# Kernel tuning notes

Measured on AMD Instinct MI355X. Metric: run time of the kernel, lower is better.

The kernel has to match this reference:

```python
import jax, jax.numpy as jnp
import numpy as np


def _hausdorff(x, y):
    # x, y: [B, C, N, D] point sets per (batch, channel); rows are points.
    x2 = jnp.sum(x * x, axis=-1)                       # [B, C, N]
    y2 = jnp.sum(y * y, axis=-1)                       # [B, C, M]
    xy = jnp.einsum('bcnd,bcmd->bcnm', x, y)           # [B, C, N, M]
    d2 = x2[..., :, None] + y2[..., None, :] - 2.0 * xy
    d = jnp.sqrt(jnp.maximum(d2, 0.0))                 # Euclidean distances
    d_fwd = jnp.max(jnp.min(d, axis=-1), axis=-1)      # max_n min_m, [B, C]
    d_bwd = jnp.max(jnp.min(d, axis=-2), axis=-1)      # max_m min_n, [B, C]
    return jnp.maximum(d_fwd, d_bwd)                   # symmetric Hausdorff [B, C]


def setup_inputs() -> dict:
    key = jax.random.key(0)
    k1, k2 = jax.random.split(key)
    B, C, H, W = 8, 3, 1024, 1024
    inp = jax.random.normal(k1, (B, C, H, W), dtype=jnp.float32)
    tgt = jax.random.normal(k2, (B, C, H, W), dtype=jnp.float32)
    return {'input': inp, 'target': tgt}


def reference(input, target):
    h = _hausdorff(input, target)        # [B, C]
    # original: sum_i mean_c(h[i]) / B == mean over (B, C)
    return jnp.mean(h)
```

## Files before the change

kernel.cpp:

```cpp
#include <hip/hip_runtime.h>
#include <math.h>

constexpr int BC = 24;
constexpr int N  = 1024;
constexpr int D  = 1024;
constexpr int TILE = 128;
constexpr int SKF = 40;

typedef short short8 __attribute__((ext_vector_type(8)));
typedef float f32x4  __attribute__((ext_vector_type(4)));

#define FINF 3.402823466e+38f


__device__ inline unsigned pk_bf16(float a, float b) {
    unsigned ua = __float_as_uint(a) + 0x8000u;
    unsigned ub = __float_as_uint(b) + 0x8000u;
    return __builtin_amdgcn_perm(ub, ua, 0x07060302);
}

__global__ __launch_bounds__(256) void prep_kernel(const float* __restrict__ X,
                                                   const float* __restrict__ Y,
                                                   unsigned short* __restrict__ Xsw,
                                                   unsigned short* __restrict__ Ysw,
                                                   float* __restrict__ xn,
                                                   float* __restrict__ yn) {
    int wave = threadIdx.x >> 6, lane = threadIdx.x & 63;
    int gtile = blockIdx.x * 4 + wave;
    bool isY = gtile >= 49152;
    int tile = isY ? gtile - 49152 : gtile;
    int bc = tile >> 11;
    int rk = tile & 2047;
    int R = rk >> 5, K = rk & 31;
    int r16 = lane & 15, quad = lane >> 4;

    const float* src = (isY ? Y : X) + ((size_t)bc * N + R * 16 + r16) * D + K * 32 + quad * 8;
    float4 a = *(const float4*)src;
    float4 b = *(const float4*)(src + 4);

    uint4 pk;
    pk.x = pk_bf16(a.x, a.y); pk.y = pk_bf16(a.z, a.w);
    pk.z = pk_bf16(b.x, b.y); pk.w = pk_bf16(b.z, b.w);
    unsigned short* dst = (isY ? Ysw : Xsw) + (size_t)tile * 512 + lane * 8;
    *(uint4*)dst = pk;

    float s = a.x * a.x + a.y * a.y + a.z * a.z + a.w * a.w
            + b.x * b.x + b.y * b.y + b.z * b.z + b.w * b.w;
    s += __shfl_xor(s, 16, 64);
    s += __shfl_xor(s, 32, 64);
    if (quad == 0)
        atomicAdd(&(isY ? yn : xn)[bc * N + R * 16 + r16], s);
}

__global__ __launch_bounds__(256) void tile_bf16_kernel(const unsigned short* __restrict__ Xsw,
                                                        const unsigned short* __restrict__ Ysw,
                                                        const float* __restrict__ xn,
                                                        const float* __restrict__ yn,
                                                        unsigned* __restrict__ rowmin,
                                                        unsigned* __restrict__ colmin) {
    int id = blockIdx.x;
    int xcd = id & 7, q = id >> 3;
    int bc = xcd * 3 + (q >> 6);
    int txy = q & 63;
    int tm = txy & 7, tn = txy >> 3;

    int wave = threadIdx.x >> 6, lane = threadIdx.x & 63;
    int wr = wave >> 1, wc = wave & 1;
    int quad = lane >> 4, tx = lane & 15;

    const unsigned short* Xb = Xsw + (size_t)bc * 2048 * 512;
    const unsigned short* Yb = Ysw + (size_t)bc * 2048 * 512;
    const unsigned short* ax = Xb + (size_t)(tn * 8 + wr * 4) * 32 * 512 + lane * 8;
    const unsigned short* by = Yb + (size_t)(tm * 8 + wc * 4) * 32 * 512 + lane * 8;

    f32x4 acc[4][4];
    #pragma unroll
    for (int i = 0; i < 4; i++)
        #pragma unroll
        for (int j = 0; j < 4; j++) acc[i][j] = (f32x4)0.f;

    short8 af[2][4], bg[2][4];
    #pragma unroll
    for (int mi = 0; mi < 4; mi++) {
        af[0][mi] = *(const short8*)(ax + mi * 16384);
        bg[0][mi] = *(const short8*)(by + mi * 16384);
    }
    #pragma unroll 2
    for (int d = 0; d < 32; d++) {
        int cur = d & 1, nxt = cur ^ 1;
        if (d < 31) {
            #pragma unroll
            for (int mi = 0; mi < 4; mi++) {
                af[nxt][mi] = *(const short8*)(ax + mi * 16384 + (d + 1) * 512);
                bg[nxt][mi] = *(const short8*)(by + mi * 16384 + (d + 1) * 512);
            }
        }
        #pragma unroll
        for (int mi = 0; mi < 4; mi++)
            #pragma unroll
            for (int mj = 0; mj < 4; mj++)
                acc[mi][mj] = __builtin_amdgcn_mfma_f32_16x16x32_bf16(af[cur][mi], bg[cur][mj], acc[mi][mj], 0, 0, 0);
    }

    int rbase = bc * N + tn * TILE + wr * 64;
    int cbase = bc * N + tm * TILE + wc * 64;
    float xnr[4][4], ynr[4];
    #pragma unroll
    for (int mi = 0; mi < 4; mi++)
        #pragma unroll
        for (int r = 0; r < 4; r++) xnr[mi][r] = xn[rbase + mi * 16 + quad * 4 + r];
    #pragma unroll
    for (int mj = 0; mj < 4; mj++) ynr[mj] = yn[cbase + mj * 16 + tx];

    float rmin[4][4], cmin[4];
    #pragma unroll
    for (int mi = 0; mi < 4; mi++)
        #pragma unroll
        for (int r = 0; r < 4; r++) rmin[mi][r] = FINF;
    #pragma unroll
    for (int mj = 0; mj < 4; mj++) cmin[mj] = FINF;

    #pragma unroll
    for (int mi = 0; mi < 4; mi++)
        #pragma unroll
        for (int mj = 0; mj < 4; mj++)
            #pragma unroll
            for (int r = 0; r < 4; r++) {
                float d2 = fmaxf(xnr[mi][r] + ynr[mj] - 2.f * acc[mi][mj][r], 0.f);
                rmin[mi][r] = fminf(rmin[mi][r], d2);
                cmin[mj]    = fminf(cmin[mj], d2);
            }

    #pragma unroll
    for (int m = 1; m < 16; m <<= 1)
        #pragma unroll
        for (int mi = 0; mi < 4; mi++)
            #pragma unroll
            for (int r = 0; r < 4; r++)
                rmin[mi][r] = fminf(rmin[mi][r], __shfl_xor(rmin[mi][r], m, 64));
    if (tx == 0) {
        #pragma unroll
        for (int mi = 0; mi < 4; mi++)
            #pragma unroll
            for (int r = 0; r < 4; r++)
                atomicMin(&rowmin[rbase + mi * 16 + quad * 4 + r], __float_as_uint(rmin[mi][r]));
    }
    #pragma unroll
    for (int m = 16; m < 64; m <<= 1)
        #pragma unroll
        for (int mj = 0; mj < 4; mj++)
            cmin[mj] = fminf(cmin[mj], __shfl_xor(cmin[mj], m, 64));
    if (quad == 0) {
        #pragma unroll
        for (int mj = 0; mj < 4; mj++)
            atomicMin(&colmin[cbase + mj * 16 + tx], __float_as_uint(cmin[mj]));
    }
}

__global__ __launch_bounds__(256) void norms_kernel(const float* __restrict__ X,
                                                    const float* __restrict__ Y,
                                                    float* __restrict__ xn,
                                                    float* __restrict__ yn) {
    int w = threadIdx.x >> 6, lane = threadIdx.x & 63;
    long rid = (long)blockIdx.x * 4 + w;
    bool isY = rid >= (long)BC * N;
    long row = isY ? rid - (long)BC * N : rid;
    const float* src = (isY ? Y : X) + row * D;
    float s = 0.f;
    #pragma unroll
    for (int q = 0; q < 4; q++) {
        float4 v = ((const float4*)src)[lane + q * 64];
        s += v.x * v.x + v.y * v.y + v.z * v.z + v.w * v.w;
    }
    #pragma unroll
    for (int m = 1; m < 64; m <<= 1) s += __shfl_xor(s, m, 64);
    if (lane == 0) (isY ? yn : xn)[row] = s;
}

__global__ __launch_bounds__(256) void tile_conv_kernel(const float* __restrict__ X,
                                                        const float* __restrict__ Y,
                                                        const float* __restrict__ xn,
                                                        const float* __restrict__ yn,
                                                        unsigned* __restrict__ rowmin,
                                                        unsigned* __restrict__ colmin) {
    __shared__ unsigned short Xs[TILE * SKF];
    __shared__ unsigned short Ys[TILE * SKF];
    int bc = blockIdx.z, tn = blockIdx.y, tm = blockIdx.x;
    const float* Xb = X + ((size_t)bc * N + (size_t)tn * TILE) * D;
    const float* Yb = Y + ((size_t)bc * N + (size_t)tm * TILE) * D;

    int t = threadIdx.x;
    int srow = t >> 3, sq = t & 7;
    int wave = t >> 6, lane = t & 63;
    int wr = wave >> 1, wc = wave & 1;
    int quad = lane >> 4, tx = lane & 15;

    f32x4 acc[4][4];
    #pragma unroll
    for (int i = 0; i < 4; i++)
        #pragma unroll
        for (int j = 0; j < 4; j++) acc[i][j] = (f32x4)0.f;

    float4 xv[4], yv[4];
    #pragma unroll
    for (int i = 0; i < 4; i++) {
        xv[i] = *(const float4*)(Xb + (size_t)(srow + i * 32) * D + sq * 4);
        yv[i] = *(const float4*)(Yb + (size_t)(srow + i * 32) * D + sq * 4);
    }

    for (int k0 = 0; k0 < D; k0 += 32) {
        __syncthreads();
        #pragma unroll
        for (int i = 0; i < 4; i++) {
            uint2 px; px.x = pk_bf16(xv[i].x, xv[i].y); px.y = pk_bf16(xv[i].z, xv[i].w);
            *(uint2*)&Xs[(srow + i * 32) * SKF + sq * 4] = px;
            uint2 py; py.x = pk_bf16(yv[i].x, yv[i].y); py.y = pk_bf16(yv[i].z, yv[i].w);
            *(uint2*)&Ys[(srow + i * 32) * SKF + sq * 4] = py;
        }
        __syncthreads();
        if (k0 + 32 < D) {
            #pragma unroll
            for (int i = 0; i < 4; i++) {
                xv[i] = *(const float4*)(Xb + (size_t)(srow + i * 32) * D + k0 + 32 + sq * 4);
                yv[i] = *(const float4*)(Yb + (size_t)(srow + i * 32) * D + k0 + 32 + sq * 4);
            }
        }
        short8 af[4], bg[4];
        #pragma unroll
        for (int mi = 0; mi < 4; mi++)
            af[mi] = *(const short8*)&Xs[(wr * 64 + mi * 16 + tx) * SKF + quad * 8];
        #pragma unroll
        for (int mj = 0; mj < 4; mj++)
            bg[mj] = *(const short8*)&Ys[(wc * 64 + mj * 16 + tx) * SKF + quad * 8];
        #pragma unroll
        for (int mi = 0; mi < 4; mi++)
            #pragma unroll
            for (int mj = 0; mj < 4; mj++)
                acc[mi][mj] = __builtin_amdgcn_mfma_f32_16x16x32_bf16(af[mi], bg[mj], acc[mi][mj], 0, 0, 0);
    }

    int rbase = bc * N + tn * TILE + wr * 64;
    int cbase = bc * N + tm * TILE + wc * 64;
    float xnr[4][4], ynr[4];
    #pragma unroll
    for (int mi = 0; mi < 4; mi++)
        #pragma unroll
        for (int r = 0; r < 4; r++) xnr[mi][r] = xn[rbase + mi * 16 + quad * 4 + r];
    #pragma unroll
    for (int mj = 0; mj < 4; mj++) ynr[mj] = yn[cbase + mj * 16 + tx];

    float rmin[4][4], cmin[4];
    #pragma unroll
    for (int mi = 0; mi < 4; mi++)
        #pragma unroll
        for (int r = 0; r < 4; r++) rmin[mi][r] = FINF;
    #pragma unroll
    for (int mj = 0; mj < 4; mj++) cmin[mj] = FINF;

    #pragma unroll
    for (int mi = 0; mi < 4; mi++)
        #pragma unroll
        for (int mj = 0; mj < 4; mj++)
            #pragma unroll
            for (int r = 0; r < 4; r++) {
                float d2 = fmaxf(xnr[mi][r] + ynr[mj] - 2.f * acc[mi][mj][r], 0.f);
                rmin[mi][r] = fminf(rmin[mi][r], d2);
                cmin[mj]    = fminf(cmin[mj], d2);
            }

    #pragma unroll
    for (int m = 1; m < 16; m <<= 1)
        #pragma unroll
        for (int mi = 0; mi < 4; mi++)
            #pragma unroll
            for (int r = 0; r < 4; r++)
                rmin[mi][r] = fminf(rmin[mi][r], __shfl_xor(rmin[mi][r], m, 64));
    if (tx == 0) {
        #pragma unroll
        for (int mi = 0; mi < 4; mi++)
            #pragma unroll
            for (int r = 0; r < 4; r++)
                atomicMin(&rowmin[rbase + mi * 16 + quad * 4 + r], __float_as_uint(rmin[mi][r]));
    }
    #pragma unroll
    for (int m = 16; m < 64; m <<= 1)
        #pragma unroll
        for (int mj = 0; mj < 4; mj++)
            cmin[mj] = fminf(cmin[mj], __shfl_xor(cmin[mj], m, 64));
    if (quad == 0) {
        #pragma unroll
        for (int mj = 0; mj < 4; mj++)
            atomicMin(&colmin[cbase + mj * 16 + tx], __float_as_uint(cmin[mj]));
    }
}

__global__ __launch_bounds__(256) void finalize_kernel(const unsigned* __restrict__ rowmin,
                                                       const unsigned* __restrict__ colmin,
                                                       float* __restrict__ out) {
    int bc = blockIdx.x;
    float v = 0.f;
    for (int i = threadIdx.x; i < N; i += 256) {
        v = fmaxf(v, __uint_as_float(rowmin[bc * N + i]));
        v = fmaxf(v, __uint_as_float(colmin[bc * N + i]));
    }
    #pragma unroll
    for (int m = 1; m < 64; m <<= 1) v = fmaxf(v, __shfl_xor(v, m, 64));
    __shared__ float ws[4];
    int lane = threadIdx.x & 63, w = threadIdx.x >> 6;
    if (lane == 0) ws[w] = v;
    __syncthreads();
    if (threadIdx.x == 0) {
        float m = fmaxf(fmaxf(ws[0], ws[1]), fmaxf(ws[2], ws[3]));
        atomicAdd(out, sqrtf(m) * (1.0f / (float)BC));
    }
}

extern "C" void kernel_launch(void* const* d_in, const int* in_sizes, int n_in,
                              void* d_out, int out_size, void* d_ws, size_t ws_size,
                              hipStream_t stream) {
    const float* X = (const float*)d_in[0];
    const float* Y = (const float*)d_in[1];
    float* out = (float*)d_out;

    unsigned* rowmin = (unsigned*)d_ws;
    unsigned* colmin = rowmin + BC * N;
    float* xn = (float*)(colmin + BC * N);
    float* yn = xn + BC * N;
    size_t head = (size_t)4 * BC * N * 4;
    size_t bf_bytes = (size_t)BC * N * D * 2;

    if (ws_size >= head + 2 * bf_bytes) {
        unsigned short* Xsw = (unsigned short*)((char*)d_ws + head);
        unsigned short* Ysw = Xsw + (size_t)BC * N * D;
        hipMemsetAsync(d_ws, 0xFF, (size_t)2 * BC * N * 4, stream);
        hipMemsetAsync(xn, 0, (size_t)2 * BC * N * 4, stream);
        hipMemsetAsync(d_out, 0, sizeof(float), stream);
        prep_kernel<<<24576, 256, 0, stream>>>(X, Y, Xsw, Ysw, xn, yn);
        tile_bf16_kernel<<<1536, 256, 0, stream>>>(Xsw, Ysw, xn, yn, rowmin, colmin);
    } else {
        hipMemsetAsync(d_ws, 0xFF, (size_t)2 * BC * N * 4, stream);
        hipMemsetAsync(d_out, 0, sizeof(float), stream);
        dim3 grid(N / TILE, N / TILE, BC);
        norms_kernel<<<2 * BC * N / 4, 256, 0, stream>>>(X, Y, xn, yn);
        tile_conv_kernel<<<grid, 256, 0, stream>>>(X, Y, xn, yn, rowmin, colmin);
    }
    finalize_kernel<<<BC, 256, 0, stream>>>(rowmin, colmin, out);
}
```

Measured before the change: 303.0 us.

## Switch staged operands from bf16 to fp8 and use fp8 MFMA for the dot products

The prep kernel now converts inputs to fp8 (packed 4 per word) instead of bf16, halving the staging buffer size and the bytes the tile kernel reads. Each wave handles four tiles with software-prefetched loads, and the grid shrinks accordingly. The tile kernel uses fp8 16x16x32 MFMA with two k-halves per 64-wide step, a simpler block-to-(bc,tile) mapping without XCD swizzle, and launch bounds requesting more occupancy. Reduced precision risks distance errors affecting the min/max Hausdorff result, and dropping the XCD-aware mapping may hurt L2 locality.

```diff
diff --git a/kernel.cpp b/kernel.cpp
--- a/kernel.cpp
+++ b/kernel.cpp
@@ -9,6 +9,7 @@
 
 typedef short short8 __attribute__((ext_vector_type(8)));
 typedef float f32x4  __attribute__((ext_vector_type(4)));
+typedef long lng2    __attribute__((ext_vector_type(2)));
 
 #define FINF 3.402823466e+38f
 
@@ -19,59 +20,88 @@
     return __builtin_amdgcn_perm(ub, ua, 0x07060302);
 }
 
+__device__ inline int pk_fp8x4(float a, float b, float c, float d) {
+    int w = __builtin_amdgcn_cvt_pk_fp8_f32(a, b, 0, false);
+    w = __builtin_amdgcn_cvt_pk_fp8_f32(c, d, w, true);
+    return w;
+}
+
 __global__ __launch_bounds__(256) void prep_kernel(const float* __restrict__ X,
                                                    const float* __restrict__ Y,
-                                                   unsigned short* __restrict__ Xsw,
-                                                   unsigned short* __restrict__ Ysw,
+                                                   unsigned char* __restrict__ Xf8,
+                                                   unsigned char* __restrict__ Yf8,
                                                    float* __restrict__ xn,
                                                    float* __restrict__ yn) {
     int wave = threadIdx.x >> 6, lane = threadIdx.x & 63;
-    int gtile = blockIdx.x * 4 + wave;
-    bool isY = gtile >= 49152;
-    int tile = isY ? gtile - 49152 : gtile;
-    int bc = tile >> 11;
-    int rk = tile & 2047;
-    int R = rk >> 5, K = rk & 31;
     int r16 = lane & 15, quad = lane >> 4;
-
-    const float* src = (isY ? Y : X) + ((size_t)bc * N + R * 16 + r16) * D + K * 32 + quad * 8;
-    float4 a = *(const float4*)src;
-    float4 b = *(const float4*)(src + 4);
-
-    uint4 pk;
-    pk.x = pk_bf16(a.x, a.y); pk.y = pk_bf16(a.z, a.w);
-    pk.z = pk_bf16(b.x, b.y); pk.w = pk_bf16(b.z, b.w);
-    unsigned short* dst = (isY ? Ysw : Xsw) + (size_t)tile * 512 + lane * 8;
-    *(uint4*)dst = pk;
-
-    float s = a.x * a.x + a.y * a.y + a.z * a.z + a.w * a.w
-            + b.x * b.x + b.y * b.y + b.z * b.z + b.w * b.w;
-    s += __shfl_xor(s, 16, 64);
-    s += __shfl_xor(s, 32, 64);
-    if (quad == 0)
-        atomicAdd(&(isY ? yn : xn)[bc * N + R * 16 + r16], s);
-}
-
-__global__ __launch_bounds__(256) void tile_bf16_kernel(const unsigned short* __restrict__ Xsw,
-                                                        const unsigned short* __restrict__ Ysw,
-                                                        const float* __restrict__ xn,
-                                                        const float* __restrict__ yn,
-                                                        unsigned* __restrict__ rowmin,
-                                                        unsigned* __restrict__ colmin) {
+    int wid = blockIdx.x * 4 + wave;
+
+    float4 c0, c1, c2, c3;
+    float4 n0, n1, n2, n3;
+
+    auto src_of = [&](int st) -> const float* {
+        bool isY = st >= 24576;
+        int s = isY ? st - 24576 : s = st;
+        s = isY ? st - 24576 : st;
+        int bc = s >> 10, rkp = s & 1023;
+        int R = rkp >> 4, Kp = rkp & 15;
+        return (isY ? Y : X) + ((size_t)bc * N + R * 16 + r16) * D + Kp * 64 + quad * 8;
+    };
+
+    {
+        const float* p = src_of(wid);
+        c0 = *(const float4*)p;        c1 = *(const float4*)(p + 4);
+        c2 = *(const float4*)(p + 32); c3 = *(const float4*)(p + 36);
+    }
+    #pragma unroll
+    for (int it = 0; it < 4; it++) {
+        int st = wid + it * 12288;
+        if (it < 3) {
+            const float* p = src_of(wid + (it + 1) * 12288);
+            n0 = *(const float4*)p;        n1 = *(const float4*)(p + 4);
+            n2 = *(const float4*)(p + 32); n3 = *(const float4*)(p + 36);
+        }
+        bool isY = st >= 24576;
+        int s = isY ? st - 24576 : st;
+        uint4 w;
+        w.x = (unsigned)pk_fp8x4(c0.x, c0.y, c0.z, c0.w);
+        w.y = (unsigned)pk_fp8x4(c1.x, c1.y, c1.z, c1.w);
+        w.z = (unsigned)pk_fp8x4(c2.x, c2.y, c2.z, c2.w);
+        w.w = (unsigned)pk_fp8x4(c3.x, c3.y, c3.z, c3.w);
+        *(uint4*)((isY ? Yf8 : Xf8) + (size_t)s * 1024 + lane * 16) = w;
+
+        float sm = c0.x*c0.x + c0.y*c0.y + c0.z*c0.z + c0.w*c0.w
+                 + c1.x*c1.x + c1.y*c1.y + c1.z*c1.z + c1.w*c1.w
+                 + c2.x*c2.x + c2.y*c2.y + c2.z*c2.z + c2.w*c2.w
+                 + c3.x*c3.x + c3.y*c3.y + c3.z*c3.z + c3.w*c3.w;
+        sm += __shfl_xor(sm, 16, 64);
+        sm += __shfl_xor(sm, 32, 64);
+        if (quad == 0) {
+            int bc = s >> 10, R = (s & 1023) >> 4;
+            atomicAdd(&(isY ? yn : xn)[bc * N + R * 16 + r16], sm);
+        }
+        c0 = n0; c1 = n1; c2 = n2; c3 = n3;
+    }
+}
+
+__global__ __launch_bounds__(256, 3) void tile_f8_kernel(const unsigned char* __restrict__ Xf8,
+                                                         const unsigned char* __restrict__ Yf8,
+                                                         const float* __restrict__ xn,
+                                                         const float* __restrict__ yn,
+                                                         unsigned* __restrict__ rowmin,
+                                                         unsigned* __restrict__ colmin) {
     int id = blockIdx.x;
-    int xcd = id & 7, q = id >> 3;
-    int bc = xcd * 3 + (q >> 6);
-    int txy = q & 63;
-    int tm = txy & 7, tn = txy >> 3;
+    int bc = id >> 6;
+    int tn = (id >> 3) & 7, tm = id & 7;
 
     int wave = threadIdx.x >> 6, lane = threadIdx.x & 63;
     int wr = wave >> 1, wc = wave & 1;
     int quad = lane >> 4, tx = lane & 15;
 
-    const unsigned short* Xb = Xsw + (size_t)bc * 2048 * 512;
-    const unsigned short* Yb = Ysw + (size_t)bc * 2048 * 512;
-    const unsigned short* ax = Xb + (size_t)(tn * 8 + wr * 4) * 32 * 512 + lane * 8;
-    const unsigned short* by = Yb + (size_t)(tm * 8 + wc * 4) * 32 * 512 + lane * 8;
+    const unsigned char* Xb = Xf8 + (size_t)bc * 1024 * 1024;
+    const unsigned char* Yb = Yf8 + (size_t)bc * 1024 * 1024;
+    const unsigned char* ax = Xb + (size_t)(tn * 8 + wr * 4) * 16 * 1024 + lane * 16;
+    const unsigned char* by = Yb + (size_t)(tm * 8 + wc * 4) * 16 * 1024 + lane * 16;
 
     f32x4 acc[4][4];
     #pragma unroll
@@ -79,27 +109,32 @@
         #pragma unroll
         for (int j = 0; j < 4; j++) acc[i][j] = (f32x4)0.f;
 
-    short8 af[2][4], bg[2][4];
+    lng2 a[2][4], b[2][4];
     #pragma unroll
     for (int mi = 0; mi < 4; mi++) {
-        af[0][mi] = *(const short8*)(ax + mi * 16384);
-        bg[0][mi] = *(const short8*)(by + mi * 16384);
-    }
-    #pragma unroll 2
-    for (int d = 0; d < 32; d++) {
-        int cur = d & 1, nxt = cur ^ 1;
-        if (d < 31) {
+        a[0][mi] = *(const lng2*)(ax + mi * 16384);
+        b[0][mi] = *(const lng2*)(by + mi * 16384);
+    }
+    #pragma unroll
+    for (int Kp = 0; Kp < 16; Kp++) {
+        int cur = Kp & 1, nxt = cur ^ 1;
+        if (Kp < 15) {
             #pragma unroll
             for (int mi = 0; mi < 4; mi++) {
-                af[nxt][mi] = *(const short8*)(ax + mi * 16384 + (d + 1) * 512);
-                bg[nxt][mi] = *(const short8*)(by + mi * 16384 + (d + 1) * 512);
+                a[nxt][mi] = *(const lng2*)(ax + mi * 16384 + (Kp + 1) * 1024);
+                b[nxt][mi] = *(const lng2*)(by + mi * 16384 + (Kp + 1) * 1024);
             }
         }
         #pragma unroll
         for (int mi = 0; mi < 4; mi++)
             #pragma unroll
             for (int mj = 0; mj < 4; mj++)
-                acc[mi][mj] = __builtin_amdgcn_mfma_f32_16x16x32_bf16(af[cur][mi], bg[cur][mj], acc[mi][mj], 0, 0, 0);
+                acc[mi][mj] = __builtin_amdgcn_mfma_f32_16x16x32_fp8_fp8(a[cur][mi].x, b[cur][mj].x, acc[mi][mj], 0, 0, 0);
+        #pragma unroll
+        for (int mi = 0; mi < 4; mi++)
+            #pragma unroll
+            for (int mj = 0; mj < 4; mj++)
+                acc[mi][mj] = __builtin_amdgcn_mfma_f32_16x16x32_fp8_fp8(a[cur][mi].y, b[cur][mj].y, acc[mi][mj], 0, 0, 0);
     }
 
     int rbase = bc * N + tn * TILE + wr * 64;
@@ -327,19 +362,18 @@
     float* xn = (float*)(colmin + BC * N);
     float* yn = xn + BC * N;
     size_t head = (size_t)4 * BC * N * 4;
-    size_t bf_bytes = (size_t)BC * N * D * 2;
-
-    if (ws_size >= head + 2 * bf_bytes) {
-        unsigned short* Xsw = (unsigned short*)((char*)d_ws + head);
-        unsigned short* Ysw = Xsw + (size_t)BC * N * D;
-        hipMemsetAsync(d_ws, 0xFF, (size_t)2 * BC * N * 4, stream);
-        hipMemsetAsync(xn, 0, (size_t)2 * BC * N * 4, stream);
-        hipMemsetAsync(d_out, 0, sizeof(float), stream);
-        prep_kernel<<<24576, 256, 0, stream>>>(X, Y, Xsw, Ysw, xn, yn);
-        tile_bf16_kernel<<<1536, 256, 0, stream>>>(Xsw, Ysw, xn, yn, rowmin, colmin);
+    size_t f8_bytes = (size_t)BC * N * D;
+
+    hipMemsetAsync(d_ws, 0xFF, (size_t)2 * BC * N * 4, stream);
+    hipMemsetAsync(xn, 0, (size_t)2 * BC * N * 4, stream);
+    hipMemsetAsync(d_out, 0, sizeof(float), stream);
+
+    if (ws_size >= head + 2 * f8_bytes) {
+        unsigned char* Xf8 = (unsigned char*)d_ws + head;
+        unsigned char* Yf8 = Xf8 + f8_bytes;
+        prep_kernel<<<3072, 256, 0, stream>>>(X, Y, Xf8, Yf8, xn, yn);
+        tile_f8_kernel<<<1536, 256, 0, stream>>>(Xf8, Yf8, xn, yn, rowmin, colmin);
     } else {
-        hipMemsetAsync(d_ws, 0xFF, (size_t)2 * BC * N * 4, stream);
-        hipMemsetAsync(d_out, 0, sizeof(float), stream);
         dim3 grid(N / TILE, N / TILE, BC);
         norms_kernel<<<2 * BC * N / 4, 256, 0, stream>>>(X, Y, xn, yn);
         tile_conv_kernel<<<grid, 256, 0, stream>>>(X, Y, xn, yn, rowmin, colmin);
```

Measured after the change: 270.3 us. -10.8%, faster.
